# Optimization experiments

Measured on AMD Instinct MI355X. Metric: run time of the kernel, lower is better.

The kernel has to match this reference:

```python
import jax, jax.numpy as jnp
import numpy as np

OUTPUT_SIZES = [1, 3, 6, 8]  # SPP pyramid -> total KV length 110

def _bounds(n, out):
    # PyTorch AdaptiveMaxPool2d bin boundaries
    return [((i * n) // out, -((-(i + 1) * n) // out)) for i in range(out)]

def adaptive_max_pool2d(x, out):
    # x: [B, C, H, W] -> [B, C, out, out]
    B, C, H, W = x.shape
    rows = jnp.stack([x[:, :, s:e, :].max(axis=2) for s, e in _bounds(H, out)], axis=2)
    return jnp.stack([rows[:, :, :, s:e].max(axis=3) for s, e in _bounds(W, out)], axis=3)

def spp(x):
    # [B, C, H, W] -> [B, C, S] with S = sum(o*o) = 110
    B, C = x.shape[:2]
    return jnp.concatenate(
        [adaptive_max_pool2d(x, o).reshape(B, C, o * o) for o in OUTPUT_SIZES], axis=2)

def conv1x1(x, w):
    # 1x1 conv, no bias: w [O, C], x [B, C, H, W]
    return jnp.einsum('oc,bchw->bohw', w, x)

def setup_inputs() -> dict:
    key = jax.random.key(0)
    ks = jax.random.split(key, 6)
    B, C, H, W = 16, 512, 64, 64
    IC = C // 2
    x = jax.random.normal(ks[0], (B, C, H, W), jnp.float32)
    y = jax.random.normal(ks[1], (B, C, H, W), jnp.float32)
    sc = 1.0 / np.sqrt(C)
    w_phi = jax.random.normal(ks[2], (IC, C), jnp.float32) * sc
    w_theta = jax.random.normal(ks[3], (IC, C), jnp.float32) * sc
    w_g = jax.random.normal(ks[4], (IC, C), jnp.float32) * sc
    w_mask = jax.random.normal(ks[5], (C, IC), jnp.float32) * (1.0 / np.sqrt(IC))
    return {"x": x, "y": y, "w_phi": w_phi, "w_theta": w_theta,
            "w_g": w_g, "w_mask": w_mask}

def reference(x, y, w_phi, w_theta, w_g, w_mask):
    B, C, H, W = x.shape
    IC = w_phi.shape[0]
    N = H * W
    # Query: [B, N, IC]
    x_phi = conv1x1(x, w_phi).reshape(B, IC, N).transpose(0, 2, 1)
    # Keys/values from SPP-pooled y: [B, IC, S] / [B, S, IC]
    y_theta = spp(conv1x1(y, w_theta))
    y_g = spp(conv1x1(y, w_g)).transpose(0, 2, 1)
    # Attention with softmax over the QUERY axis (dim=1), as in the source
    attn = jax.nn.softmax(jnp.einsum('bnc,bcs->bns', x_phi, y_theta), axis=1)
    agg = jnp.einsum('bns,bsc->bnc', attn, y_g)          # [B, N, IC]
    agg = agg.transpose(0, 2, 1).reshape(B, IC, H, W)     # [B, IC, H, W]
    mask = conv1x1(agg, w_mask)                           # [B, C, H, W]
    return mask + x
```

## Files before the change

kernel.cpp:

```cpp
#include <hip/hip_runtime.h>

#define DI __device__ __forceinline__

typedef __attribute__((ext_vector_type(8))) __bf16 bf16x8;
typedef __attribute__((ext_vector_type(4))) float f32x4;

DI unsigned short f2bf(float x) {
  union { float f; unsigned u; } v; v.f = x;
  unsigned r = v.u + 0x7fffu + ((v.u >> 16) & 1u);
  return (unsigned short)(r >> 16);
}
DI float bf2f(unsigned short h) {
  union { unsigned u; float f; } v; v.u = ((unsigned)h) << 16;
  return v.f;
}
DI unsigned pack2(float a, float b) {
  return (unsigned)f2bf(a) | (((unsigned)f2bf(b)) << 16);
}

DI void gl_lds16(const void* g, void* l) {
  __builtin_amdgcn_global_load_lds(
      (const __attribute__((address_space(1))) void*)g,
      (__attribute__((address_space(3))) void*)l, 16, 0, 0);
}

__global__ __launch_bounds__(256) void p0_transpose(
    const float* __restrict__ src, unsigned short* __restrict__ dst)
{
  const int n0 = blockIdx.x * 64, c0 = blockIdx.y * 64, b = blockIdx.z;
  const int tid = threadIdx.x;
  __shared__ float T[64 * 65];
  #pragma unroll
  for (int p = 0; p < 4; ++p) {
    int r = p * 16 + (tid >> 4);
    int n4 = (tid & 15) << 2;
    *(float4*)&T[r * 65 + n4] =
        *(const float4*)(src + ((size_t)(b * 512 + c0 + r)) * 4096 + n0 + n4);
  }
  __syncthreads();
  int n = tid >> 2, cc = (tid & 3) * 16;
  unsigned u[8];
  #pragma unroll
  for (int j = 0; j < 16; j += 2)
    u[j >> 1] = pack2(T[(cc + j) * 65 + n], T[(cc + j + 1) * 65 + n]);
  unsigned short* d = dst + ((size_t)(b * 4096 + n0 + n)) * 512 + c0 + cc;
  *(uint4*)(d) = make_uint4(u[0], u[1], u[2], u[3]);
  *(uint4*)(d + 8) = make_uint4(u[4], u[5], u[6], u[7]);
}

__constant__ int c_RS[18] = {0, 0,21,42, 0,10,21,32,42,53, 0,8,16,24,32,40,48,56};
__constant__ int c_RE[18] = {64, 22,43,64, 11,22,32,43,54,64, 8,16,24,32,40,48,56,64};

__global__ __launch_bounds__(256) void k1f_conv_pool(
    const unsigned short* __restrict__ yT, const float* __restrict__ w_theta,
    const float* __restrict__ w_g, unsigned short* __restrict__ Rbuf)
{
  const int tid = threadIdx.x;
  const int id = blockIdx.x;
  const int tile = (id & 7) * 16 + (id >> 3);
  const int mb = (tile & 3) * 128;
  const int nbt = tile >> 2;
  const int nb = nbt * 128;
  const int b  = blockIdx.y;
  const int lane = tid & 63, wv = tid >> 6;
  const int wm = (wv & 1) * 64, wn = (wv >> 1) * 64;
  const int l15 = lane & 15, l4 = lane >> 4;

  __shared__ __align__(16) char smem[33280];
  unsigned short* As = (unsigned short*)smem;
  unsigned short* Bs = (unsigned short*)(smem + 8192);
  float* P = (float*)smem;

  f32x4 acc[4][4];
  #pragma unroll
  for (int i = 0; i < 4; ++i)
    #pragma unroll
    for (int j = 0; j < 4; ++j) acc[i][j] = f32x4{0.f, 0.f, 0.f, 0.f};

  for (int kb = 0; kb < 512; kb += 32) {
    #pragma unroll
    for (int p = 0; p < 2; ++p) {
      int chunk = (wv * 2 + p) * 64 + lane;
      int row = chunk >> 2, c16 = chunk & 3;
      gl_lds16(yT + ((size_t)(b * 4096 + nb + row)) * 512 + kb + c16 * 8,
               Bs + (wv * 2 + p) * 512);
    }
    #pragma unroll
    for (int j = 0; j < 4; ++j) {
      int flat = tid + 256 * j;
      int row = flat >> 3, c4 = (flat & 7) << 2;
      int og = mb + row;
      const float* wr = (og < 256) ? (w_theta + (size_t)og * 512)
                                   : (w_g + (size_t)(og - 256) * 512);
      float4 v = *(const float4*)(wr + kb + c4);
      uint2 u; u.x = pack2(v.x, v.y); u.y = pack2(v.z, v.w);
      *(uint2*)&As[row * 32 + c4] = u;
    }
    __syncthreads();
    bf16x8 af[4], bfr[4];
    #pragma unroll
    for (int i = 0; i < 4; ++i)
      af[i] = *(const bf16x8*)&As[(wm + i * 16 + l15) * 32 + l4 * 8];
    #pragma unroll
    for (int j = 0; j < 4; ++j)
      bfr[j] = *(const bf16x8*)&Bs[(wn + j * 16 + l15) * 32 + l4 * 8];
    #pragma unroll
    for (int i = 0; i < 4; ++i)
      #pragma unroll
      for (int j = 0; j < 4; ++j)
        acc[i][j] = __builtin_amdgcn_mfma_f32_16x16x32_bf16(af[i], bfr[j], acc[i][j], 0, 0, 0);
    __syncthreads();
  }

  const int hloc = wv >> 1;
  #pragma unroll
  for (int pass = 0; pass < 2; ++pass) {
    __syncthreads();
    if (hloc == pass) {
      #pragma unroll
      for (int i = 0; i < 4; ++i)
        #pragma unroll
        for (int j = 0; j < 4; ++j)
          #pragma unroll
          for (int r = 0; r < 4; ++r)
            P[(wm + i * 16 + l4 * 4 + r) * 65 + j * 16 + l15] = acc[i][j][r];
    }
    __syncthreads();
    const int o = tid & 127;
    size_t rbase = (((size_t)(b * 64 + nbt * 2 + pass)) * 18) * 512 + mb + o;
    if (tid < 128) {
      float b0 = -3.4e38f, b1 = b0, b2 = b0, b3 = b0;
      #pragma unroll
      for (int w = 0; w < 64; ++w) {
        float v = P[o * 65 + w];
        b0 = fmaxf(b0, v);
        if (w < 22) b1 = fmaxf(b1, v);
        if (w >= 21 && w < 43) b2 = fmaxf(b2, v);
        if (w >= 42) b3 = fmaxf(b3, v);
      }
      Rbuf[rbase]           = f2bf(b0);
      Rbuf[rbase + 512]     = f2bf(b1);
      Rbuf[rbase + 2 * 512] = f2bf(b2);
      Rbuf[rbase + 3 * 512] = f2bf(b3);
    } else {
      float s6[6], s8[8];
      #pragma unroll
      for (int i = 0; i < 6; ++i) s6[i] = -3.4e38f;
      #pragma unroll
      for (int i = 0; i < 8; ++i) s8[i] = -3.4e38f;
      constexpr int R6S[6] = {0, 10, 21, 32, 42, 53};
      constexpr int R6E[6] = {11, 22, 32, 43, 54, 64};
      #pragma unroll
      for (int w = 0; w < 64; ++w) {
        float v = P[o * 65 + w];
        #pragma unroll
        for (int i = 0; i < 6; ++i)
          if (w >= R6S[i] && w < R6E[i]) s6[i] = fmaxf(s6[i], v);
        s8[w >> 3] = fmaxf(s8[w >> 3], v);
      }
      #pragma unroll
      for (int i = 0; i < 6; ++i) Rbuf[rbase + (size_t)(4 + i) * 512] = f2bf(s6[i]);
      #pragma unroll
      for (int i = 0; i < 8; ++i) Rbuf[rbase + (size_t)(10 + i) * 512] = f2bf(s8[i]);
    }
  }
}

__global__ __launch_bounds__(256) void k2_pool_final(
    const unsigned short* __restrict__ Rbuf, float* __restrict__ Pt,
    float* __restrict__ Pg)
{
  const int s = blockIdx.x, b = blockIdx.y, tid = threadIdx.x;
  size_t obase = ((size_t)(b * 128) + s) * 256 + tid;
  if (s >= 110) { Pt[obase] = 0.f; Pg[obase] = 0.f; return; }
  int he, wb;
  if (s == 0)      { he = 0; wb = 0; }
  else if (s < 10) { int i = s - 1;  he = 1 + i / 3;  wb = 1 + i % 3; }
  else if (s < 46) { int i = s - 10; he = 4 + i / 6;  wb = 4 + i % 6; }
  else             { int i = s - 46; he = 10 + i / 8; wb = 10 + i % 8; }
  float m0 = -3.4e38f, m1 = -3.4e38f;
  int e = c_RE[he];
  for (int h = c_RS[he]; h < e; ++h) {
    const unsigned short* r = Rbuf + (((size_t)(b * 64 + h)) * 18 + wb) * 512;
    m0 = fmaxf(m0, bf2f(r[tid]));
    m1 = fmaxf(m1, bf2f(r[tid + 256]));
  }
  Pt[obase] = m0;
  Pg[obase] = m1;
}

__global__ __launch_bounds__(256) void k3_kmat(
    const float* __restrict__ Pt, const float* __restrict__ w_phi,
    unsigned short* __restrict__ Kth, unsigned short* __restrict__ Ktl)
{
  const int ct = blockIdx.x, b = blockIdx.y, tid = threadIdx.x;
  const int tx = tid & 15, ty = tid >> 4;
  const int c0 = tx * 4, s0 = ty * 8;
  __shared__ float Ls[128 * 64];
  __shared__ float Ws[64 * 68];
  float acc[8][4] = {};
  for (int kc = 0; kc < 256; kc += 64) {
    #pragma unroll
    for (int j = 0; j < 8; ++j) {
      int flat = tid + 256 * j;
      int row = flat >> 4, k4 = (flat & 15) << 2;
      *(float4*)&Ls[row * 64 + k4] =
          *(const float4*)(Pt + ((size_t)(b * 128) + row) * 256 + kc + k4);
    }
    #pragma unroll
    for (int j = 0; j < 4; ++j) {
      int flat = tid + 256 * j;
      int row = flat >> 4, c4 = (flat & 15) << 2;
      *(float4*)&Ws[row * 68 + c4] =
          *(const float4*)(w_phi + (size_t)(kc + row) * 512 + ct * 64 + c4);
    }
    __syncthreads();
    for (int k = 0; k < 64; k += 4) {
      float4 wv[4];
      #pragma unroll
      for (int kk = 0; kk < 4; ++kk) wv[kk] = *(const float4*)&Ws[(k + kk) * 68 + c0];
      #pragma unroll
      for (int i = 0; i < 8; ++i) {
        float4 a = *(const float4*)&Ls[(s0 + i) * 64 + k];
        const float* ap = (const float*)&a;
        #pragma unroll
        for (int kk = 0; kk < 4; ++kk) {
          const float* wp = (const float*)&wv[kk];
          acc[i][0] += ap[kk] * wp[0];
          acc[i][1] += ap[kk] * wp[1];
          acc[i][2] += ap[kk] * wp[2];
          acc[i][3] += ap[kk] * wp[3];
        }
      }
    }
    __syncthreads();
  }
  #pragma unroll
  for (int i = 0; i < 8; ++i) {
    unsigned short hi[4]; float lo[4];
    #pragma unroll
    for (int j = 0; j < 4; ++j) { hi[j] = f2bf(acc[i][j]); lo[j] = acc[i][j] - bf2f(hi[j]); }
    size_t base = ((size_t)(b * 128) + s0 + i) * 512 + ct * 64 + c0;
    uint2 uh; uh.x = (unsigned)hi[0] | ((unsigned)hi[1] << 16);
    uh.y = (unsigned)hi[2] | ((unsigned)hi[3] << 16);
    uint2 ul; ul.x = pack2(lo[0], lo[1]); ul.y = pack2(lo[2], lo[3]);
    *(uint2*)&Kth[base] = uh;
    *(uint2*)&Ktl[base] = ul;
  }
}

__global__ __launch_bounds__(256) void k3_vmat(
    const float* __restrict__ Pg, const float* __restrict__ w_mask,
    float* __restrict__ V)
{
  const int ot = blockIdx.x, b = blockIdx.y, tid = threadIdx.x;
  const int tx = tid & 15, ty = tid >> 4;
  const int o0 = ty * 4;
  __shared__ float Ws[64 * 64];
  __shared__ float Ps[128 * 68];
  float acc[4][8] = {};
  for (int kc = 0; kc < 256; kc += 64) {
    #pragma unroll
    for (int j = 0; j < 4; ++j) {
      int flat = tid + 256 * j;
      int row = flat >> 4, k4 = (flat & 15) << 2;
      *(float4*)&Ws[row * 64 + k4] =
          *(const float4*)(w_mask + (size_t)(ot * 64 + row) * 256 + kc + k4);
    }
    #pragma unroll
    for (int j = 0; j < 8; ++j) {
      int flat = tid + 256 * j;
      int row = flat >> 4, k4 = (flat & 15) << 2;
      *(float4*)&Ps[row * 68 + k4] =
          *(const float4*)(Pg + ((size_t)(b * 128) + row) * 256 + kc + k4);
    }
    __syncthreads();
    for (int k = 0; k < 64; k += 4) {
      float4 wv[4];
      #pragma unroll
      for (int i = 0; i < 4; ++i) wv[i] = *(const float4*)&Ws[(o0 + i) * 64 + k];
      #pragma unroll
      for (int jj = 0; jj < 8; ++jj) {
        float4 pv = *(const float4*)&Ps[(tx + 16 * jj) * 68 + k];
        const float* pp = (const float*)&pv;
        #pragma unroll
        for (int i = 0; i < 4; ++i) {
          const float* wp = (const float*)&wv[i];
          #pragma unroll
          for (int kk = 0; kk < 4; ++kk) acc[i][jj] += wp[kk] * pp[kk];
        }
      }
    }
    __syncthreads();
  }
  #pragma unroll
  for (int i = 0; i < 4; ++i)
    #pragma unroll
    for (int jj = 0; jj < 8; ++jj)
      V[((size_t)(b * 512) + ot * 64 + o0 + i) * 128 + tx + 16 * jj] = acc[i][jj];
}

__global__ __launch_bounds__(256) void k4_scores(
    const unsigned short* __restrict__ xT, const unsigned short* __restrict__ Kth,
    const unsigned short* __restrict__ Ktl, float* __restrict__ scores)
{
  const int tid = threadIdx.x;
  const int nb = blockIdx.x * 128;
  const int b = blockIdx.y;
  const int lane = tid & 63, wv = tid >> 6;
  const int wm = (wv & 1) * 64, wn = (wv >> 1) * 64;
  const int l15 = lane & 15, l4 = lane >> 4;
  __shared__ __align__(16) unsigned short Ah[128 * 32];
  __shared__ __align__(16) unsigned short Al[128 * 32];
  __shared__ __align__(16) unsigned short Bs[128 * 32];
  f32x4 acc[4][4];
  #pragma unroll
  for (int i = 0; i < 4; ++i)
    #pragma unroll
    for (int j = 0; j < 4; ++j) acc[i][j] = f32x4{0.f, 0.f, 0.f, 0.f};

  for (int kb = 0; kb < 512; kb += 32) {
    #pragma unroll
    for (int p = 0; p < 2; ++p) {
      int chunk = (wv * 2 + p) * 64 + lane;
      int row = chunk >> 2, c16 = chunk & 3;
      size_t g = ((size_t)(b * 128) + row) * 512 + kb + c16 * 8;
      gl_lds16(Kth + g, Ah + (wv * 2 + p) * 512);
      gl_lds16(Ktl + g, Al + (wv * 2 + p) * 512);
      gl_lds16(xT + ((size_t)(b * 4096 + nb + row)) * 512 + kb + c16 * 8,
               Bs + (wv * 2 + p) * 512);
    }
    __syncthreads();
    bf16x8 ah[4], al[4], bfr[4];
    #pragma unroll
    for (int i = 0; i < 4; ++i) {
      ah[i] = *(const bf16x8*)&Ah[(wm + i * 16 + l15) * 32 + l4 * 8];
      al[i] = *(const bf16x8*)&Al[(wm + i * 16 + l15) * 32 + l4 * 8];
    }
    #pragma unroll
    for (int j = 0; j < 4; ++j)
      bfr[j] = *(const bf16x8*)&Bs[(wn + j * 16 + l15) * 32 + l4 * 8];
    #pragma unroll
    for (int i = 0; i < 4; ++i)
      #pragma unroll
      for (int j = 0; j < 4; ++j) {
        acc[i][j] = __builtin_amdgcn_mfma_f32_16x16x32_bf16(ah[i], bfr[j], acc[i][j], 0, 0, 0);
        acc[i][j] = __builtin_amdgcn_mfma_f32_16x16x32_bf16(al[i], bfr[j], acc[i][j], 0, 0, 0);
      }
    __syncthreads();
  }
  #pragma unroll
  for (int i = 0; i < 4; ++i)
    #pragma unroll
    for (int j = 0; j < 4; ++j)
      #pragma unroll
      for (int r = 0; r < 4; ++r)
        scores[((size_t)(b * 128) + wm + i * 16 + l4 * 4 + r) * 4096 + nb + wn + j * 16 + l15] =
            acc[i][j][r];
}

__global__ __launch_bounds__(256) void k5_stats(
    const float* __restrict__ scores, float* __restrict__ mbuf,
    float* __restrict__ lbuf)
{
  const int s = blockIdx.x, b = blockIdx.y, tid = threadIdx.x;
  if (s >= 110) {
    if (tid == 0) { mbuf[b * 128 + s] = 0.f; lbuf[b * 128 + s] = 0.f; }
    return;
  }
  const float* row = scores + ((size_t)(b * 128) + s) * 4096;
  float4 v[4];
  float m = -3.4e38f;
  #pragma unroll
  for (int j = 0; j < 4; ++j) {
    v[j] = *(const float4*)(row + (tid + 256 * j) * 4);
    m = fmaxf(m, fmaxf(fmaxf(v[j].x, v[j].y), fmaxf(v[j].z, v[j].w)));
  }
  #pragma unroll
  for (int off = 32; off > 0; off >>= 1) m = fmaxf(m, __shfl_down(m, off));
  __shared__ float red[8];
  if ((tid & 63) == 0) red[tid >> 6] = m;
  __syncthreads();
  float mm = fmaxf(fmaxf(red[0], red[1]), fmaxf(red[2], red[3]));
  float sum = 0.f;
  #pragma unroll
  for (int j = 0; j < 4; ++j)
    sum += __expf(v[j].x - mm) + __expf(v[j].y - mm) +
           __expf(v[j].z - mm) + __expf(v[j].w - mm);
  #pragma unroll
  for (int off = 32; off > 0; off >>= 1) sum += __shfl_down(sum, off);
  if ((tid & 63) == 0) red[4 + (tid >> 6)] = sum;
  __syncthreads();
  if (tid == 0) {
    float S = red[4] + red[5] + red[6] + red[7];
    mbuf[b * 128 + s] = mm;
    lbuf[b * 128 + s] = 1.f / S;
  }
}

__global__ __launch_bounds__(256) void k5e_expT(
    const float* __restrict__ scores, const float* __restrict__ mbuf,
    unsigned short* __restrict__ Eb)
{
  const int nt = blockIdx.x, b = blockIdx.y, tid = threadIdx.x;
  __shared__ float L[128 * 68];
  __shared__ float sm[128];
  if (tid < 128) sm[tid] = mbuf[b * 128 + tid];
  #pragma unroll
  for (int j = 0; j < 8; ++j) {
    int flat = tid + 256 * j;
    int s = flat >> 4, n4 = (flat & 15) << 2;
    *(float4*)&L[s * 68 + n4] =
        *(const float4*)(scores + ((size_t)(b * 128) + s) * 4096 + nt * 64 + n4);
  }
  __syncthreads();
  int n = tid >> 2, sq = (tid & 3) * 32;
  unsigned ub[16];
  #pragma unroll
  for (int k = 0; k < 32; k += 2) {
    float e0 = __expf(L[(sq + k) * 68 + n] - sm[sq + k]);
    float e1 = __expf(L[(sq + k + 1) * 68 + n] - sm[sq + k + 1]);
    ub[k >> 1] = pack2(e0, e1);
  }
  uint4* dst = (uint4*)(Eb + ((size_t)(b * 4096) + nt * 64 + n) * 128 + sq);
  #pragma unroll
  for (int j = 0; j < 4; ++j)
    dst[j] = make_uint4(ub[4 * j], ub[4 * j + 1], ub[4 * j + 2], ub[4 * j + 3]);
}

__global__ __launch_bounds__(256) void k6_out(
    const unsigned short* __restrict__ Eb, const float* __restrict__ V,
    const float* __restrict__ lbuf, const float* __restrict__ x,
    float* __restrict__ out)
{
  const int tid = threadIdx.x;
  const int nb = blockIdx.x * 128;
  const int mb = blockIdx.y * 128;
  const int b = blockIdx.z;
  const int lane = tid & 63, wv = tid >> 6;
  const int wm = (wv & 1) * 64, wn = (wv >> 1) * 64;
  const int l15 = lane & 15, l4 = lane >> 4;
  __shared__ unsigned short Ah[128 * 72];
  __shared__ unsigned short Bt[128 * 72];
  __shared__ float sl[128];
  if (tid < 128) sl[tid] = lbuf[b * 128 + tid];

  f32x4 acc[4][4];
  #pragma unroll
  for (int i = 0; i < 4; ++i)
    #pragma unroll
    for (int j = 0; j < 4; ++j) acc[i][j] = f32x4{0.f, 0.f, 0.f, 0.f};

  for (int kc = 0; kc < 128; kc += 64) {
    __syncthreads();
    #pragma unroll
    for (int j = 0; j < 8; ++j) {
      int flat = tid + 256 * j;
      int row = flat >> 4, s4 = (flat & 15) << 2;
      float4 v = *(const float4*)(V + ((size_t)(b * 512) + mb + row) * 128 + kc + s4);
      v.x *= sl[kc + s4]; v.y *= sl[kc + s4 + 1];
      v.z *= sl[kc + s4 + 2]; v.w *= sl[kc + s4 + 3];
      uint2 u; u.x = pack2(v.x, v.y); u.y = pack2(v.z, v.w);
      *(uint2*)&Ah[row * 72 + s4] = u;
    }
    #pragma unroll
    for (int j = 0; j < 4; ++j) {
      int flat = tid + 256 * j;
      int n = flat >> 3, s8 = (flat & 7) << 3;
      *(uint4*)&Bt[n * 72 + s8] =
          *(const uint4*)(Eb + ((size_t)(b * 4096) + nb + n) * 128 + kc + s8);
    }
    __syncthreads();
    #pragma unroll
    for (int kb = 0; kb < 64; kb += 32) {
      bf16x8 af[4], bfr[4];
      #pragma unroll
      for (int i = 0; i < 4; ++i)
        af[i] = *(const bf16x8*)&Ah[(wm + i * 16 + l15) * 72 + kb + l4 * 8];
      #pragma unroll
      for (int j = 0; j < 4; ++j)
        bfr[j] = *(const bf16x8*)&Bt[(wn + j * 16 + l15) * 72 + kb + l4 * 8];
      #pragma unroll
      for (int i = 0; i < 4; ++i)
        #pragma unroll
        for (int j = 0; j < 4; ++j)
          acc[i][j] = __builtin_amdgcn_mfma_f32_16x16x32_bf16(af[i], bfr[j], acc[i][j], 0, 0, 0);
    }
  }
  #pragma unroll
  for (int i = 0; i < 4; ++i)
    #pragma unroll
    for (int j = 0; j < 4; ++j)
      #pragma unroll
      for (int r = 0; r < 4; ++r) {
        int o = mb + wm + i * 16 + l4 * 4 + r;
        size_t idx = ((size_t)(b * 512) + o) * 4096 + nb + wn + j * 16 + l15;
        out[idx] = acc[i][j][r] + x[idx];
      }
}

extern "C" void kernel_launch(void* const* d_in, const int* in_sizes, int n_in,
                              void* d_out, int out_size, void* d_ws, size_t ws_size,
                              hipStream_t stream)
{
  (void)in_sizes; (void)n_in; (void)out_size; (void)ws_size;
  const float* x       = (const float*)d_in[0];
  const float* y       = (const float*)d_in[1];
  const float* w_phi   = (const float*)d_in[2];
  const float* w_theta = (const float*)d_in[3];
  const float* w_g     = (const float*)d_in[4];
  const float* w_mask  = (const float*)d_in[5];
  float* out = (float*)d_out;

  char* ws = (char*)d_ws;
  unsigned short* yT = (unsigned short*)ws;
  unsigned short* xT = yT;
  char* B0 = ws + 67108864;
  unsigned short* Rbuf = (unsigned short*)B0;
  float* scores = (float*)B0;
  unsigned short* Eb = (unsigned short*)(B0 + 33554432);
  float* V = (float*)(B0 + 50331648);
  char* C0 = B0 + 54525952;
  float* Pt = (float*)C0;
  float* Pg = (float*)(C0 + 2097152);
  unsigned short* Kth = (unsigned short*)(C0 + 4194304);
  unsigned short* Ktl = (unsigned short*)(C0 + 6291456);
  float* mbuf = (float*)(C0 + 8388608);
  float* lbuf = (float*)(C0 + 8396800);

  p0_transpose<<<dim3(64, 8, 16), 256, 0, stream>>>(y, yT);
  k1f_conv_pool<<<dim3(128, 16), 256, 0, stream>>>(yT, w_theta, w_g, Rbuf);
  k2_pool_final<<<dim3(128, 16), 256, 0, stream>>>(Rbuf, Pt, Pg);
  k3_kmat<<<dim3(8, 16), 256, 0, stream>>>(Pt, w_phi, Kth, Ktl);
  k3_vmat<<<dim3(8, 16), 256, 0, stream>>>(Pg, w_mask, V);
  p0_transpose<<<dim3(64, 8, 16), 256, 0, stream>>>(x, xT);
  k4_scores<<<dim3(32, 16), 256, 0, stream>>>(xT, Kth, Ktl, scores);
  k5_stats<<<dim3(128, 16), 256, 0, stream>>>(scores, mbuf, lbuf);
  k5e_expT<<<dim3(64, 16), 256, 0, stream>>>(scores, mbuf, Eb);
  k6_out<<<dim3(32, 4, 16), 256, 0, stream>>>(Eb, V, lbuf, x, out);
}
```

Baseline: 552.9 us.

## Preconvert weights to bf16, fuse K/V matmuls, async LDS loads in output GEMM

Adds a small kernel that converts w_theta and w_g to bf16 once, so the conv+pool GEMM can stream weight tiles straight into LDS with global_load_lds instead of converting fp32 on every tile. The K and V projection kernels are merged into one launch split on blockIdx.z, and V is now stored as bf16. The softmax normalisation factor moves from the V operand into the exp kernel. The output GEMM then loads both operands with direct-to-LDS async copies into unpadded split buffers. This cuts launches, fp32 traffic and per-tile conversion work, at the cost of an extra tiny launch and possible LDS bank conflicts from the unpadded layout.

```diff
diff --git a/kernel.cpp b/kernel.cpp
--- a/kernel.cpp
+++ b/kernel.cpp
@@ -22,6 +22,20 @@
   __builtin_amdgcn_global_load_lds(
       (const __attribute__((address_space(1))) void*)g,
       (__attribute__((address_space(3))) void*)l, 16, 0, 0);
+}
+
+__global__ __launch_bounds__(256) void pw_conv(
+    const float* __restrict__ w_theta, const float* __restrict__ w_g,
+    unsigned short* __restrict__ wTG)
+{
+  int e = (blockIdx.x * 256 + threadIdx.x) * 8;
+  const float* src = (e < 131072) ? (w_theta + e) : (w_g + (e - 131072));
+  float4 a = *(const float4*)src;
+  float4 c = *(const float4*)(src + 4);
+  uint4 u;
+  u.x = pack2(a.x, a.y); u.y = pack2(a.z, a.w);
+  u.z = pack2(c.x, c.y); u.w = pack2(c.z, c.w);
+  *(uint4*)(wTG + e) = u;
 }
 
 __global__ __launch_bounds__(256) void p0_transpose(
@@ -52,8 +66,8 @@
 __constant__ int c_RE[18] = {64, 22,43,64, 11,22,32,43,54,64, 8,16,24,32,40,48,56,64};
 
 __global__ __launch_bounds__(256) void k1f_conv_pool(
-    const unsigned short* __restrict__ yT, const float* __restrict__ w_theta,
-    const float* __restrict__ w_g, unsigned short* __restrict__ Rbuf)
+    const unsigned short* __restrict__ yT, const unsigned short* __restrict__ wTG,
+    unsigned short* __restrict__ Rbuf)
 {
   const int tid = threadIdx.x;
   const int id = blockIdx.x;
@@ -82,19 +96,10 @@
     for (int p = 0; p < 2; ++p) {
       int chunk = (wv * 2 + p) * 64 + lane;
       int row = chunk >> 2, c16 = chunk & 3;
+      gl_lds16(wTG + ((size_t)(mb + row)) * 512 + kb + c16 * 8,
+               As + (wv * 2 + p) * 512);
       gl_lds16(yT + ((size_t)(b * 4096 + nb + row)) * 512 + kb + c16 * 8,
                Bs + (wv * 2 + p) * 512);
-    }
-    #pragma unroll
-    for (int j = 0; j < 4; ++j) {
-      int flat = tid + 256 * j;
-      int row = flat >> 3, c4 = (flat & 7) << 2;
-      int og = mb + row;
-      const float* wr = (og < 256) ? (w_theta + (size_t)og * 512)
-                                   : (w_g + (size_t)(og - 256) * 512);
-      float4 v = *(const float4*)(wr + kb + c4);
-      uint2 u; u.x = pack2(v.x, v.y); u.y = pack2(v.z, v.w);
-      *(uint2*)&As[row * 32 + c4] = u;
     }
     __syncthreads();
     bf16x8 af[4], bfr[4];
@@ -189,115 +194,117 @@
   Pg[obase] = m1;
 }
 
-__global__ __launch_bounds__(256) void k3_kmat(
-    const float* __restrict__ Pt, const float* __restrict__ w_phi,
-    unsigned short* __restrict__ Kth, unsigned short* __restrict__ Ktl)
-{
-  const int ct = blockIdx.x, b = blockIdx.y, tid = threadIdx.x;
+__global__ __launch_bounds__(256) void k3_fused(
+    const float* __restrict__ Pt, const float* __restrict__ Pg,
+    const float* __restrict__ w_phi, const float* __restrict__ w_mask,
+    unsigned short* __restrict__ Kth, unsigned short* __restrict__ Ktl,
+    unsigned short* __restrict__ Vb)
+{
+  __shared__ __align__(16) char sm3[51200];
+  const int tid = threadIdx.x;
   const int tx = tid & 15, ty = tid >> 4;
-  const int c0 = tx * 4, s0 = ty * 8;
-  __shared__ float Ls[128 * 64];
-  __shared__ float Ws[64 * 68];
-  float acc[8][4] = {};
-  for (int kc = 0; kc < 256; kc += 64) {
-    #pragma unroll
-    for (int j = 0; j < 8; ++j) {
-      int flat = tid + 256 * j;
-      int row = flat >> 4, k4 = (flat & 15) << 2;
-      *(float4*)&Ls[row * 64 + k4] =
-          *(const float4*)(Pt + ((size_t)(b * 128) + row) * 256 + kc + k4);
-    }
-    #pragma unroll
-    for (int j = 0; j < 4; ++j) {
-      int flat = tid + 256 * j;
-      int row = flat >> 4, c4 = (flat & 15) << 2;
-      *(float4*)&Ws[row * 68 + c4] =
-          *(const float4*)(w_phi + (size_t)(kc + row) * 512 + ct * 64 + c4);
-    }
-    __syncthreads();
-    for (int k = 0; k < 64; k += 4) {
-      float4 wv[4];
-      #pragma unroll
-      for (int kk = 0; kk < 4; ++kk) wv[kk] = *(const float4*)&Ws[(k + kk) * 68 + c0];
-      #pragma unroll
-      for (int i = 0; i < 8; ++i) {
-        float4 a = *(const float4*)&Ls[(s0 + i) * 64 + k];
-        const float* ap = (const float*)&a;
-        #pragma unroll
-        for (int kk = 0; kk < 4; ++kk) {
-          const float* wp = (const float*)&wv[kk];
-          acc[i][0] += ap[kk] * wp[0];
-          acc[i][1] += ap[kk] * wp[1];
-          acc[i][2] += ap[kk] * wp[2];
-          acc[i][3] += ap[kk] * wp[3];
+  const int b = blockIdx.y;
+  if (blockIdx.z == 0) {
+    const int ct = blockIdx.x;
+    const int c0 = tx * 4, s0 = ty * 8;
+    float* Ls = (float*)sm3;
+    float* Ws = Ls + 128 * 64;
+    float acc[8][4] = {};
+    for (int kc = 0; kc < 256; kc += 64) {
+      #pragma unroll
+      for (int j = 0; j < 8; ++j) {
+        int flat = tid + 256 * j;
+        int row = flat >> 4, k4 = (flat & 15) << 2;
+        *(float4*)&Ls[row * 64 + k4] =
+            *(const float4*)(Pt + ((size_t)(b * 128) + row) * 256 + kc + k4);
+      }
+      #pragma unroll
+      for (int j = 0; j < 4; ++j) {
+        int flat = tid + 256 * j;
+        int row = flat >> 4, c4 = (flat & 15) << 2;
+        *(float4*)&Ws[row * 68 + c4] =
+            *(const float4*)(w_phi + (size_t)(kc + row) * 512 + ct * 64 + c4);
+      }
+      __syncthreads();
+      for (int k = 0; k < 64; k += 4) {
+        float4 wv[4];
+        #pragma unroll
+        for (int kk = 0; kk < 4; ++kk) wv[kk] = *(const float4*)&Ws[(k + kk) * 68 + c0];
+        #pragma unroll
+        for (int i = 0; i < 8; ++i) {
+          float4 a = *(const float4*)&Ls[(s0 + i) * 64 + k];
+          const float* ap = (const float*)&a;
+          #pragma unroll
+          for (int kk = 0; kk < 4; ++kk) {
+            const float* wp = (const float*)&wv[kk];
+            acc[i][0] += ap[kk] * wp[0];
+            acc[i][1] += ap[kk] * wp[1];
+            acc[i][2] += ap[kk] * wp[2];
+            acc[i][3] += ap[kk] * wp[3];
+          }
         }
       }
-    }
-    __syncthreads();
-  }
-  #pragma unroll
-  for (int i = 0; i < 8; ++i) {
-    unsigned short hi[4]; float lo[4];
-    #pragma unroll
-    for (int j = 0; j < 4; ++j) { hi[j] = f2bf(acc[i][j]); lo[j] = acc[i][j] - bf2f(hi[j]); }
-    size_t base = ((size_t)(b * 128) + s0 + i) * 512 + ct * 64 + c0;
-    uint2 uh; uh.x = (unsigned)hi[0] | ((unsigned)hi[1] << 16);
-    uh.y = (unsigned)hi[2] | ((unsigned)hi[3] << 16);
-    uint2 ul; ul.x = pack2(lo[0], lo[1]); ul.y = pack2(lo[2], lo[3]);
-    *(uint2*)&Kth[base] = uh;
-    *(uint2*)&Ktl[base] = ul;
-  }
-}
-
-__global__ __launch_bounds__(256) void k3_vmat(
-    const float* __restrict__ Pg, const float* __restrict__ w_mask,
-    float* __restrict__ V)
-{
-  const int ot = blockIdx.x, b = blockIdx.y, tid = threadIdx.x;
-  const int tx = tid & 15, ty = tid >> 4;
-  const int o0 = ty * 4;
-  __shared__ float Ws[64 * 64];
-  __shared__ float Ps[128 * 68];
-  float acc[4][8] = {};
-  for (int kc = 0; kc < 256; kc += 64) {
-    #pragma unroll
-    for (int j = 0; j < 4; ++j) {
-      int flat = tid + 256 * j;
-      int row = flat >> 4, k4 = (flat & 15) << 2;
-      *(float4*)&Ws[row * 64 + k4] =
-          *(const float4*)(w_mask + (size_t)(ot * 64 + row) * 256 + kc + k4);
-    }
-    #pragma unroll
-    for (int j = 0; j < 8; ++j) {
-      int flat = tid + 256 * j;
-      int row = flat >> 4, k4 = (flat & 15) << 2;
-      *(float4*)&Ps[row * 68 + k4] =
-          *(const float4*)(Pg + ((size_t)(b * 128) + row) * 256 + kc + k4);
-    }
-    __syncthreads();
-    for (int k = 0; k < 64; k += 4) {
-      float4 wv[4];
-      #pragma unroll
-      for (int i = 0; i < 4; ++i) wv[i] = *(const float4*)&Ws[(o0 + i) * 64 + k];
-      #pragma unroll
-      for (int jj = 0; jj < 8; ++jj) {
-        float4 pv = *(const float4*)&Ps[(tx + 16 * jj) * 68 + k];
-        const float* pp = (const float*)&pv;
-        #pragma unroll
-        for (int i = 0; i < 4; ++i) {
-          const float* wp = (const float*)&wv[i];
+      __syncthreads();
+    }
+    #pragma unroll
+    for (int i = 0; i < 8; ++i) {
+      unsigned short hi[4]; float lo[4];
+      #pragma unroll
+      for (int j = 0; j < 4; ++j) { hi[j] = f2bf(acc[i][j]); lo[j] = acc[i][j] - bf2f(hi[j]); }
+      size_t base = ((size_t)(b * 128) + s0 + i) * 512 + ct * 64 + c0;
+      uint2 uh; uh.x = (unsigned)hi[0] | ((unsigned)hi[1] << 16);
+      uh.y = (unsigned)hi[2] | ((unsigned)hi[3] << 16);
+      uint2 ul; ul.x = pack2(lo[0], lo[1]); ul.y = pack2(lo[2], lo[3]);
+      *(uint2*)&Kth[base] = uh;
+      *(uint2*)&Ktl[base] = ul;
+    }
+  } else {
+    const int ot = blockIdx.x;
+    const int o0 = ty * 4;
+    float* Ws = (float*)sm3;
+    float* Ps = Ws + 64 * 64;
+    float acc[4][8] = {};
+    for (int kc = 0; kc < 256; kc += 64) {
+      #pragma unroll
+      for (int j = 0; j < 4; ++j) {
+        int flat = tid + 256 * j;
+        int row = flat >> 4, k4 = (flat & 15) << 2;
+        *(float4*)&Ws[row * 64 + k4] =
+            *(const float4*)(w_mask + (size_t)(ot * 64 + row) * 256 + kc + k4);
+      }
+      #pragma unroll
+      for (int j = 0; j < 8; ++j) {
+        int flat = tid + 256 * j;
+        int row = flat >> 4, k4 = (flat & 15) << 2;
+        *(float4*)&Ps[row * 68 + k4] =
+            *(const float4*)(Pg + ((size_t)(b * 128) + row) * 256 + kc + k4);
+      }
+      __syncthreads();
+      for (int k = 0; k < 64; k += 4) {
+        float4 wv[4];
+        #pragma unroll
+        for (int i = 0; i < 4; ++i) wv[i] = *(const float4*)&Ws[(o0 + i) * 64 + k];
+        #pragma unroll
+        for (int jj = 0; jj < 8; ++jj) {
+          float4 pv = *(const float4*)&Ps[(tx + 16 * jj) * 68 + k];
+          const float* pp = (const float*)&pv;
           #pragma unroll
-          for (int kk = 0; kk < 4; ++kk) acc[i][jj] += wp[kk] * pp[kk];
+          for (int i = 0; i < 4; ++i) {
+            const float* wp = (const float*)&wv[i];
+            #pragma unroll
+            for (int kk = 0; kk < 4; ++kk) acc[i][jj] += wp[kk] * pp[kk];
+          }
         }
       }
-    }
-    __syncthreads();
-  }
-  #pragma unroll
-  for (int i = 0; i < 4; ++i)
-    #pragma unroll
-    for (int jj = 0; jj < 8; ++jj)
-      V[((size_t)(b * 512) + ot * 64 + o0 + i) * 128 + tx + 16 * jj] = acc[i][jj];
+      __syncthreads();
+    }
+    #pragma unroll
+    for (int i = 0; i < 4; ++i)
+      #pragma unroll
+      for (int jj = 0; jj < 8; ++jj)
+        Vb[((size_t)(b * 512) + ot * 64 + o0 + i) * 128 + tx + 16 * jj] =
+            f2bf(acc[i][jj]);
+  }
 }
 
 __global__ __launch_bounds__(256) void k4_scores(
@@ -400,12 +407,12 @@
 
 __global__ __launch_bounds__(256) void k5e_expT(
     const float* __restrict__ scores, const float* __restrict__ mbuf,
-    unsigned short* __restrict__ Eb)
+    const float* __restrict__ lbuf, unsigned short* __restrict__ Eb)
 {
   const int nt = blockIdx.x, b = blockIdx.y, tid = threadIdx.x;
   __shared__ float L[128 * 68];
-  __shared__ float sm[128];
-  if (tid < 128) sm[tid] = mbuf[b * 128 + tid];
+  __shared__ float sm[128], sl[128];
+  if (tid < 128) { sm[tid] = mbuf[b * 128 + tid]; sl[tid] = lbuf[b * 128 + tid]; }
   #pragma unroll
   for (int j = 0; j < 8; ++j) {
     int flat = tid + 256 * j;
@@ -418,8 +425,8 @@
   unsigned ub[16];
   #pragma unroll
   for (int k = 0; k < 32; k += 2) {
-    float e0 = __expf(L[(sq + k) * 68 + n] - sm[sq + k]);
-    float e1 = __expf(L[(sq + k + 1) * 68 + n] - sm[sq + k + 1]);
+    float e0 = __expf(L[(sq + k) * 68 + n] - sm[sq + k]) * sl[sq + k];
+    float e1 = __expf(L[(sq + k + 1) * 68 + n] - sm[sq + k + 1]) * sl[sq + k + 1];
     ub[k >> 1] = pack2(e0, e1);
   }
   uint4* dst = (uint4*)(Eb + ((size_t)(b * 4096) + nt * 64 + n) * 128 + sq);
@@ -429,9 +436,8 @@
 }
 
 __global__ __launch_bounds__(256) void k6_out(
-    const unsigned short* __restrict__ Eb, const float* __restrict__ V,
-    const float* __restrict__ lbuf, const float* __restrict__ x,
-    float* __restrict__ out)
+    const unsigned short* __restrict__ Eb, const unsigned short* __restrict__ Vb,
+    const float* __restrict__ x, float* __restrict__ out)
 {
   const int tid = threadIdx.x;
   const int nb = blockIdx.x * 128;
@@ -440,10 +446,10 @@
   const int lane = tid & 63, wv = tid >> 6;
   const int wm = (wv & 1) * 64, wn = (wv >> 1) * 64;
   const int l15 = lane & 15, l4 = lane >> 4;
-  __shared__ unsigned short Ah[128 * 72];
-  __shared__ unsigned short Bt[128 * 72];
-  __shared__ float sl[128];
-  if (tid < 128) sl[tid] = lbuf[b * 128 + tid];
+  __shared__ __align__(16) unsigned short A0[128 * 32];
+  __shared__ __align__(16) unsigned short A1[128 * 32];
+  __shared__ __align__(16) unsigned short B0[128 * 32];
+  __shared__ __align__(16) unsigned short B1[128 * 32];
 
   f32x4 acc[4][4];
   #pragma unroll
@@ -452,40 +458,36 @@
     for (int j = 0; j < 4; ++j) acc[i][j] = f32x4{0.f, 0.f, 0.f, 0.f};
 
   for (int kc = 0; kc < 128; kc += 64) {
-    __syncthreads();
-    #pragma unroll
-    for (int j = 0; j < 8; ++j) {
-      int flat = tid + 256 * j;
-      int row = flat >> 4, s4 = (flat & 15) << 2;
-      float4 v = *(const float4*)(V + ((size_t)(b * 512) + mb + row) * 128 + kc + s4);
-      v.x *= sl[kc + s4]; v.y *= sl[kc + s4 + 1];
-      v.z *= sl[kc + s4 + 2]; v.w *= sl[kc + s4 + 3];
-      uint2 u; u.x = pack2(v.x, v.y); u.y = pack2(v.z, v.w);
-      *(uint2*)&Ah[row * 72 + s4] = u;
-    }
-    #pragma unroll
-    for (int j = 0; j < 4; ++j) {
-      int flat = tid + 256 * j;
-      int n = flat >> 3, s8 = (flat & 7) << 3;
-      *(uint4*)&Bt[n * 72 + s8] =
-          *(const uint4*)(Eb + ((size_t)(b * 4096) + nb + n) * 128 + kc + s8);
-    }
-    __syncthreads();
-    #pragma unroll
-    for (int kb = 0; kb < 64; kb += 32) {
+    #pragma unroll
+    for (int p = 0; p < 2; ++p) {
+      int chunk = (wv * 2 + p) * 64 + lane;
+      int row = chunk >> 2, c16 = chunk & 3;
+      size_t ga = ((size_t)(b * 512) + mb + row) * 128 + kc + c16 * 8;
+      gl_lds16(Vb + ga,      A0 + (wv * 2 + p) * 512);
+      gl_lds16(Vb + ga + 32, A1 + (wv * 2 + p) * 512);
+      size_t gb = ((size_t)(b * 4096) + nb + row) * 128 + kc + c16 * 8;
+      gl_lds16(Eb + gb,      B0 + (wv * 2 + p) * 512);
+      gl_lds16(Eb + gb + 32, B1 + (wv * 2 + p) * 512);
+    }
+    __syncthreads();
+    #pragma unroll
+    for (int h = 0; h < 2; ++h) {
+      const unsigned short* Ak = h ? A1 : A0;
+      const unsigned short* Bk = h ? B1 : B0;
       bf16x8 af[4], bfr[4];
       #pragma unroll
       for (int i = 0; i < 4; ++i)
-        af[i] = *(const bf16x8*)&Ah[(wm + i * 16 + l15) * 72 + kb + l4 * 8];
+        af[i] = *(const bf16x8*)&Ak[(wm + i * 16 + l15) * 32 + l4 * 8];
       #pragma unroll
       for (int j = 0; j < 4; ++j)
-        bfr[j] = *(const bf16x8*)&Bt[(wn + j * 16 + l15) * 72 + kb + l4 * 8];
+        bfr[j] = *(const bf16x8*)&Bk[(wn + j * 16 + l15) * 32 + l4 * 8];
       #pragma unroll
       for (int i = 0; i < 4; ++i)
         #pragma unroll
         for (int j = 0; j < 4; ++j)
           acc[i][j] = __builtin_amdgcn_mfma_f32_16x16x32_bf16(af[i], bfr[j], acc[i][j], 0, 0, 0);
     }
+    __syncthreads();
   }
   #pragma unroll
   for (int i = 0; i < 4; ++i)
@@ -519,7 +521,8 @@
   unsigned short* Rbuf = (unsigned short*)B0;
   float* scores = (float*)B0;
   unsigned short* Eb = (unsigned short*)(B0 + 33554432);
-  float* V = (float*)(B0 + 50331648);
+  unsigned short* wTG = (unsigned short*)(B0 + 50331648);
+  unsigned short* Vb  = (unsigned short*)(B0 + 50331648);
   char* C0 = B0 + 54525952;
   float* Pt = (float*)C0;
   float* Pg = (float*)(C0 + 2097152);
@@ -528,14 +531,14 @@
   float* mbuf = (float*)(C0 + 8388608);
   float* lbuf = (float*)(C0 + 8396800);
 
+  pw_conv<<<dim3(128), 256, 0, stream>>>(w_theta, w_g, wTG);
   p0_transpose<<<dim3(64, 8, 16), 256, 0, stream>>>(y, yT);
-  k1f_conv_pool<<<dim3(128, 16), 256, 0, stream>>>(yT, w_theta, w_g, Rbuf);
+  k1f_conv_pool<<<dim3(128, 16), 256, 0, stream>>>(yT, wTG, Rbuf);
   k2_pool_final<<<dim3(128, 16), 256, 0, stream>>>(Rbuf, Pt, Pg);
-  k3_kmat<<<dim3(8, 16), 256, 0, stream>>>(Pt, w_phi, Kth, Ktl);
-  k3_vmat<<<dim3(8, 16), 256, 0, stream>>>(Pg, w_mask, V);
+  k3_fused<<<dim3(8, 16, 2), 256, 0, stream>>>(Pt, Pg, w_phi, w_mask, Kth, Ktl, Vb);
   p0_transpose<<<dim3(64, 8, 16), 256, 0, stream>>>(x, xT);
   k4_scores<<<dim3(32, 16), 256, 0, stream>>>(xT, Kth, Ktl, scores);
   k5_stats<<<dim3(128, 16), 256, 0, stream>>>(scores, mbuf, lbuf);
-  k5e_expT<<<dim3(64, 16), 256, 0, stream>>>(scores, mbuf, Eb);
-  k6_out<<<dim3(32, 4, 16), 256, 0, stream>>>(Eb, V, lbuf, x, out);
-}
+  k5e_expT<<<dim3(64, 16), 256, 0, stream>>>(scores, mbuf, lbuf, Eb);
+  k6_out<<<dim3(32, 4, 16), 256, 0, stream>>>(Eb, Vb, x, out);
+}
```

Result: faster. 521.4 us (-5.7%).
